# Kernel tuning notes

Hardware: AMD Instinct MI355X
Metric: run time of the kernel (lower is better)

## Reference

```python
import jax, jax.numpy as jnp
import numpy as np

EPS = 1e-12  # layer_norm_eps

def gelu_bert(x):
    return 0.5 * x * (1.0 + jax.lax.erf(x / jnp.sqrt(2.0).astype(x.dtype)))

def sym_normalize(A):
    # D^{-1/2} A D^{-1/2} via outer-product scaling (algebraic form of diag matmuls)
    d = A.sum(-1)                      # [B,N] row sums
    dinv = jnp.power(d, -0.5)
    return A * dinv[..., :, None] * dinv[..., None, :]

def layernorm(x, g, b):
    mu = x.mean(-1, keepdims=True)
    var = ((x - mu) ** 2).mean(-1, keepdims=True)
    return (x - mu) * jax.lax.rsqrt(var + EPS) * g + b

def gcn(x, adj, w1, w2):
    x = jax.nn.relu(jnp.matmul(adj, x @ w1))   # [B,N,I]
    x = jax.nn.relu(jnp.matmul(adj, x @ w2))   # [B,N,H]
    return x

def setup_inputs() -> dict:
    B, N, H, I = 8, 1024, 768, 3072
    key = jax.random.key(0)
    ks = jax.random.split(key, 20)
    s = 0.02
    inp = {
        'nodes': jax.random.normal(ks[0], (B, N, H), jnp.float32),
        'graphs': jax.random.uniform(ks[1], (B, 2, N, N), jnp.float32),
        'gcn1_w1': jax.random.normal(ks[2], (H, I), jnp.float32) * s,
        'gcn1_w2': jax.random.normal(ks[3], (I, H), jnp.float32) * s,
        'gcn2_w1': jax.random.normal(ks[4], (H, I), jnp.float32) * s,
        'gcn2_w2': jax.random.normal(ks[5], (I, H), jnp.float32) * s,
        'exp1_w': jax.random.normal(ks[6], (H, I), jnp.float32) * s,
        'exp1_b': jnp.zeros((I,), jnp.float32),
        'col1_w': jax.random.normal(ks[7], (I, H), jnp.float32) * s,
        'col1_b': jnp.zeros((H,), jnp.float32),
        'exp2_w': jax.random.normal(ks[8], (H, I), jnp.float32) * s,
        'exp2_b': jnp.zeros((I,), jnp.float32),
        'col2_w': jax.random.normal(ks[9], (I, H), jnp.float32) * s,
        'col2_b': jnp.zeros((H,), jnp.float32),
        'gate_w': jax.random.normal(ks[10], (4 * H, H), jnp.float32) * s,
        'gate_b': jnp.zeros((H,), jnp.float32),
        'ln1_g': jnp.ones((H,), jnp.float32),
        'ln1_b': jnp.zeros((H,), jnp.float32),
        'ln2_g': jnp.ones((H,), jnp.float32),
        'ln2_b': jnp.zeros((H,), jnp.float32),
    }
    return inp

def reference(nodes, graphs, gcn1_w1, gcn1_w2, gcn2_w1, gcn2_w2,
              exp1_w, exp1_b, col1_w, col1_b, exp2_w, exp2_b, col2_w, col2_b,
              gate_w, gate_b, ln1_g, ln1_b, ln2_g, ln2_b):
    adj1 = sym_normalize(graphs[:, 0])   # [B,N,N]
    adj2 = sym_normalize(graphs[:, 1])
    g1 = gcn(nodes, adj1, gcn1_w1, gcn1_w2)  # [B,N,H]
    g2 = gcn(nodes, adj2, gcn2_w1, gcn2_w2)
    # FFN + residual + LN (dropout = identity at eval)
    g1 = gelu_bert(g1 @ exp1_w + exp1_b) @ col1_w + col1_b
    g1 = layernorm(nodes + g1, ln1_g, ln1_b)
    g2 = gelu_bert(g2 @ exp2_w + exp2_b) @ col2_w + col2_b
    g2 = layernorm(nodes + g2, ln2_g, ln2_b)
    gate_in = jnp.concatenate((g1, g2, g1 + g2, g1 - g2), axis=2)  # [B,N,4H]
    gate = jax.nn.sigmoid(gate_in @ gate_w + gate_b)
    return gate * g1 + (1.0 - gate) * g2
```

## Files before the change

kernel.cpp:

```cpp
#include <hip/hip_runtime.h>
#include <hip/hip_bf16.h>

typedef __bf16 b8v __attribute__((ext_vector_type(8)));
typedef float  f4v __attribute__((ext_vector_type(4)));
typedef unsigned long long ull;

#define AS3(p)  ((__attribute__((address_space(3))) void*)(p))
#define AS1C(p) ((const __attribute__((address_space(1))) void*)(p))

template<int EPI>
__global__ __launch_bounds__(512, 2) void gemm256(
    const __hip_bfloat16* __restrict__ A,  long long sA,
    const __hip_bfloat16* __restrict__ Bt, long long sBg, long long sBb, int ldB,
    __hip_bfloat16* __restrict__ C, long long sC, int ldC,
    const float* __restrict__ bias0, const float* __restrict__ bias1, int K)
{
  const int bz = blockIdx.z;
  A  += (long long)bz * sA;
  Bt += (long long)(bz >> 3) * sBg + (long long)(bz & 7) * sBb;
  const float* __restrict__ bias = (bz & 1) ? bias1 : bias0;

  __shared__ __hip_bfloat16 As[4][8192];
  __shared__ __hip_bfloat16 Bs[4][8192];

  const int tid  = threadIdx.x;
  const int lane = tid & 63;
  const int wave = tid >> 6;
  const int wr = wave >> 2;
  const int wc = wave & 3;
  const int lm = lane & 15;
  const int kq = lane >> 4;

  const long long m0 = (long long)blockIdx.x * 256;
  const long long n0 = (long long)blockIdx.y * 256;

  const int sr  = tid >> 2;
  const int gch = (tid & 3) ^ ((tid >> 3) & 3);
  const __hip_bfloat16* aRow = A  + (m0 + sr) * (long long)K   + gch * 8;
  const __hip_bfloat16* bRow = Bt + (n0 + sr) * (long long)ldB + gch * 8;
  const int ld0 = tid * 8;

  auto stage = [&](int t) {
    const int buf = t & 3, k0 = t * 32;
    __builtin_amdgcn_global_load_lds(AS1C(aRow + k0),               AS3(&As[buf][ld0]),        16, 0, 0);
    __builtin_amdgcn_global_load_lds(AS1C(aRow + k0 + 128LL * K),   AS3(&As[buf][4096 + ld0]), 16, 0, 0);
    __builtin_amdgcn_global_load_lds(AS1C(bRow + k0),               AS3(&Bs[buf][ld0]),        16, 0, 0);
    __builtin_amdgcn_global_load_lds(AS1C(bRow + k0 + 128LL * ldB), AS3(&Bs[buf][4096 + ld0]), 16, 0, 0);
  };

  const int NK = K >> 5;
  stage(0); stage(1); stage(2);

  f4v acc[8][4];
  const f4v fz = {0.0f, 0.0f, 0.0f, 0.0f};
#pragma unroll
  for (int i = 0; i < 8; i++)
#pragma unroll
    for (int j = 0; j < 4; j++) acc[i][j] = fz;

  const int swz  = (kq ^ ((lm >> 1) & 3)) * 8;
  const int aoff = (wr * 128 + lm) * 32 + swz;
  const int boff = (wc * 64  + lm) * 32 + swz;

#define GBODY(T, VM)                                                          \
  {                                                                           \
    asm volatile("s_waitcnt vmcnt(" #VM ")" ::: "memory");                    \
    __builtin_amdgcn_s_barrier();                                             \
    __builtin_amdgcn_sched_barrier(0);                                        \
    if ((T) + 3 < NK) stage((T) + 3);                                         \
    const int buf_ = (T) & 3;                                                 \
    b8v af[8], bf[4];                                                         \
    _Pragma("unroll")                                                         \
    for (int i = 0; i < 8; i++) af[i] = *(const b8v*)(&As[buf_][aoff + i * 512]); \
    _Pragma("unroll")                                                         \
    for (int j = 0; j < 4; j++) bf[j] = *(const b8v*)(&Bs[buf_][boff + j * 512]); \
    __builtin_amdgcn_s_setprio(1);                                            \
    _Pragma("unroll")                                                         \
    for (int i = 0; i < 8; i++)                                               \
      _Pragma("unroll")                                                       \
      for (int j = 0; j < 4; j++)                                             \
        acc[i][j] = __builtin_amdgcn_mfma_f32_16x16x32_bf16(bf[j], af[i], acc[i][j], 0, 0, 0); \
    __builtin_amdgcn_s_setprio(0);                                            \
  }

  for (int t = 0; t < NK - 2; ++t) GBODY(t, 8)
  GBODY(NK - 2, 4)
  GBODY(NK - 1, 0)
#undef GBODY

#pragma unroll
  for (int i = 0; i < 8; i++) {
    const long long row = m0 + wr * 128 + i * 16 + lm;
#pragma unroll
    for (int j = 0; j < 4; j++) {
      const int colb = (int)n0 + wc * 64 + j * 16 + kq * 4;
      float v[4];
#pragma unroll
      for (int rg = 0; rg < 4; rg++) v[rg] = acc[i][j][rg];
      if constexpr (EPI == 1) {
#pragma unroll
        for (int rg = 0; rg < 4; rg++) v[rg] = fmaxf(v[rg], 0.0f);
      }
      if constexpr (EPI == 2) {
        const float4 b4 = *(const float4*)(bias + colb);
        const float* bb = (const float*)&b4;
#pragma unroll
        for (int rg = 0; rg < 4; rg++) {
          float x = v[rg] + bb[rg];
          v[rg] = 0.5f * x * (1.0f + erff(x * 0.70710678118654752f));
        }
      }
      union { __hip_bfloat16 h[4]; ull u; } P;
#pragma unroll
      for (int rg = 0; rg < 4; rg++) P.h[rg] = __float2bfloat16(v[rg]);
      *(ull*)(C + (long long)bz * sC + row * (long long)ldC + colb) = P.u;
    }
  }
}

template<int EPI, int OBF, int ORIENT, int MP>
__global__ __launch_bounds__(256) void gemm_bt(
    const __hip_bfloat16* __restrict__ A,  long long sA,
    const __hip_bfloat16* __restrict__ Bt, long long sBg, long long sBb, int ldB,
    void* __restrict__ Cv, long long sC, int ldC,
    const float* __restrict__ bias0, const float* __restrict__ bias1,
    const __hip_bfloat16* __restrict__ gcat, int K)
{
  const int bz = blockIdx.z;
  A  += (long long)bz * sA;
  Bt += (long long)(bz >> 3) * sBg + (long long)(bz & 7) * sBb;
  const float* __restrict__ bias = (bz & 1) ? bias1 : bias0;

  __shared__ __hip_bfloat16 As[128 * 32];
  __shared__ __hip_bfloat16 Bs[128 * 32];

  const int tid  = threadIdx.x;
  const int lane = tid & 63;
  const int wave = tid >> 6;

  const long long mBase = (long long)blockIdx.x * (MP * 128);
  const long long n0    = (long long)blockIdx.y * 128;

  const int r  = tid >> 2;
  const int kc = (tid & 3) ^ ((r >> 2) & 3);
  const __hip_bfloat16* aRow = A  + (mBase + r) * (long long)K   + kc * 8;
  const __hip_bfloat16* bRow = Bt + (n0 + r)    * (long long)ldB + kc * 8;

  const int wm = (wave & 1) * 64;
  const int wn = (wave >> 1) * 64;
  const int lm = lane & 15;
  const int kq = lane >> 4;

  const int sw   = (lm >> 2) & 3;
  const int aOff = (wm + lm) * 32 + (kq ^ sw) * 8;
  const int bOff = (wn + lm) * 32 + (kq ^ sw) * 8;

  auto stage = [&](long long aoff, int k0) {
    const __hip_bfloat16* a = aRow + aoff + k0;
    const __hip_bfloat16* b = bRow + k0;
    __builtin_amdgcn_global_load_lds(AS1C(a),              AS3(As + tid * 8),        16, 0, 0);
    __builtin_amdgcn_global_load_lds(AS1C(a + 64LL * K),   AS3(As + 2048 + tid * 8), 16, 0, 0);
    __builtin_amdgcn_global_load_lds(AS1C(b),              AS3(Bs + tid * 8),        16, 0, 0);
    __builtin_amdgcn_global_load_lds(AS1C(b + 64LL * ldB), AS3(Bs + 2048 + tid * 8), 16, 0, 0);
  };

  stage(0, 0);

  const f4v fzero = {0.0f, 0.0f, 0.0f, 0.0f};
  char* Cb = (char*)Cv;

  for (int p = 0; p < MP; ++p) {
    const long long aoff = (long long)p * 128 * K;

    f4v acc[4][4];
#pragma unroll
    for (int i = 0; i < 4; i++)
#pragma unroll
      for (int j = 0; j < 4; j++) acc[i][j] = fzero;

    for (int k0 = 0; k0 < K; k0 += 32) {
      __syncthreads();

      b8v af[4], bf[4];
#pragma unroll
      for (int i = 0; i < 4; i++) af[i] = *(const b8v*)(As + aOff + i * 16 * 32);
#pragma unroll
      for (int j = 0; j < 4; j++) bf[j] = *(const b8v*)(Bs + bOff + j * 16 * 32);

      __syncthreads();

      if (k0 + 32 < K)            stage(aoff, k0 + 32);
      else if (MP > 1 && p + 1 < MP) stage(aoff + 128LL * K, 0);

#pragma unroll
      for (int i = 0; i < 4; i++)
#pragma unroll
        for (int j = 0; j < 4; j++) {
          if constexpr (ORIENT == 0)
            acc[i][j] = __builtin_amdgcn_mfma_f32_16x16x32_bf16(bf[j], af[i], acc[i][j], 0, 0, 0);
          else
            acc[i][j] = __builtin_amdgcn_mfma_f32_16x16x32_bf16(af[i], bf[j], acc[i][j], 0, 0, 0);
        }
    }

    const long long m0 = mBase + (long long)p * 128;
#pragma unroll
    for (int i = 0; i < 4; i++) {
#pragma unroll
      for (int j = 0; j < 4; j++) {
        float v[4];
#pragma unroll
        for (int rg = 0; rg < 4; rg++) v[rg] = acc[i][j][rg];

        if constexpr (ORIENT == 0) {
          const long long row  = m0 + wm + i * 16 + lm;
          const int       colb = (int)n0 + wn + j * 16 + kq * 4;
          if constexpr (EPI == 1) {
#pragma unroll
            for (int rg = 0; rg < 4; rg++) v[rg] = fmaxf(v[rg], 0.0f);
          }
          if constexpr (EPI == 2) {
            const float4 b4 = *(const float4*)(bias + colb);
            const float* bb = (const float*)&b4;
#pragma unroll
            for (int rg = 0; rg < 4; rg++) {
              float x = v[rg] + bb[rg];
              v[rg] = 0.5f * x * (1.0f + erff(x * 0.70710678118654752f));
            }
          }
          const long long base = bz * sC + row * (long long)ldC + colb;
          if constexpr (EPI == 3) {
            const float4 b4 = *(const float4*)(bias0 + colb);
            const float* bb = (const float*)&b4;
            union { __hip_bfloat16 h[4]; ull u; } g1, g2;
            g1.u = *(const ull*)(gcat + row * 1536 + colb);
            g2.u = *(const ull*)(gcat + row * 1536 + 768 + colb);
            float o[4];
#pragma unroll
            for (int rg = 0; rg < 4; rg++) {
              const float s = 1.0f / (1.0f + expf(-(v[rg] + bb[rg])));
              o[rg] = s * __bfloat162float(g1.h[rg]) +
                      (1.0f - s) * __bfloat162float(g2.h[rg]);
            }
            *(float4*)(Cb + base * 4) = *(const float4*)o;
          } else if constexpr (OBF) {
            union { __hip_bfloat16 h[4]; ull u; } P;
#pragma unroll
            for (int rg = 0; rg < 4; rg++) P.h[rg] = __float2bfloat16(v[rg]);
            *(ull*)(Cb + base * 2) = P.u;
          } else {
            *(float4*)(Cb + base * 4) = *(const float4*)v;
          }
        } else {
          const long long crow = n0 + wn + j * 16 + lm;
          const long long mb   = m0 + wm + i * 16 + kq * 4;
          if constexpr (EPI == 1) {
#pragma unroll
            for (int rg = 0; rg < 4; rg++) v[rg] = fmaxf(v[rg], 0.0f);
          }
          const long long base = bz * sC + crow * (long long)ldC + mb;
          if constexpr (OBF) {
            union { __hip_bfloat16 h[4]; ull u; } P;
#pragma unroll
            for (int rg = 0; rg < 4; rg++) P.h[rg] = __float2bfloat16(v[rg]);
            *(ull*)(Cb + base * 2) = P.u;
          } else {
            *(float4*)(Cb + base * 4) = *(const float4*)v;
          }
        }
      }
    }
  }
}

__global__ __launch_bounds__(256) void rowsum_dinv(const float* __restrict__ g,
                                                   float* __restrict__ dinv)
{
  const int wave = threadIdx.x >> 6, lane = threadIdx.x & 63;
  const long long row = (long long)blockIdx.x * 4 + wave;
  const float4* p = (const float4*)(g + row * 1024);
  float s = 0.0f;
#pragma unroll
  for (int k = 0; k < 4; k++) {
    float4 v = p[lane + k * 64];
    s += v.x + v.y + v.z + v.w;
  }
#pragma unroll
  for (int o = 32; o > 0; o >>= 1) s += __shfl_down(s, o);
  if (lane == 0) dinv[row] = 1.0f / sqrtf(s);
}

__global__ __launch_bounds__(256) void scale_adj(const float* __restrict__ g,
                                                 const float* __restrict__ dinv,
                                                 __hip_bfloat16* __restrict__ out)
{
  const long long t = (long long)blockIdx.x * 256 + threadIdx.x;
  const long long e = t * 4;
  const int m = (int)(e >> 20);
  const int i = (int)((e >> 10) & 1023);
  const int j = (int)(e & 1023);
  const float4 v  = *(const float4*)(g + e);
  const float  di = dinv[m * 1024 + i];
  const float4 dj = *(const float4*)(dinv + m * 1024 + j);
  const int om = (m & 1) * 8 + (m >> 1);
  union { __hip_bfloat16 h[4]; ull u; } r;
  r.h[0] = __float2bfloat16(v.x * di * dj.x);
  r.h[1] = __float2bfloat16(v.y * di * dj.y);
  r.h[2] = __float2bfloat16(v.z * di * dj.z);
  r.h[3] = __float2bfloat16(v.w * di * dj.w);
  *(ull*)(out + ((long long)om << 20) + (long long)i * 1024 + j) = r.u;
}

template<typename TIN>
__global__ void transpose_conv(const TIN* __restrict__ in, __hip_bfloat16* __restrict__ out,
                               int R, int C, long long sIn, long long sOut)
{
  __shared__ __hip_bfloat16 tile[32][33];
  in  += (long long)blockIdx.z * sIn;
  out += (long long)blockIdx.z * sOut;
  const int c0 = blockIdx.x * 32, r0 = blockIdx.y * 32;
  const int tx = threadIdx.x, ty = threadIdx.y;
#pragma unroll
  for (int i = 0; i < 32; i += 8)
    tile[ty + i][tx] = __float2bfloat16((float)in[(long long)(r0 + ty + i) * C + c0 + tx]);
  __syncthreads();
#pragma unroll
  for (int i = 0; i < 32; i += 8)
    out[(long long)(c0 + ty + i) * R + r0 + tx] = tile[tx][ty + i];
}

__global__ __launch_bounds__(256) void ln_residual2(
    const float* __restrict__ nodes, const __hip_bfloat16* __restrict__ V,
    const float* __restrict__ colb0, const float* __restrict__ colb1,
    const float* __restrict__ lng0,  const float* __restrict__ lng1,
    const float* __restrict__ lnb0,  const float* __restrict__ lnb1,
    __hip_bfloat16* __restrict__ gcat)
{
  const long long row = blockIdx.x;
  const int g = (int)(row >> 13);
  const long long rr = row & 8191;
  const float* __restrict__ colb = g ? colb1 : colb0;
  const float* __restrict__ lng  = g ? lng1  : lng0;
  const float* __restrict__ lnb  = g ? lnb1  : lnb0;
  const int t = threadIdx.x;
  const long long nbase = rr * 768;
  const long long vbase = row * 768;
  float x[3]; float s = 0.0f, ss = 0.0f;
#pragma unroll
  for (int i = 0; i < 3; i++) {
    const int c = t + i * 256;
    const float v = nodes[nbase + c] + __bfloat162float(V[vbase + c]) + colb[c];
    x[i] = v; s += v; ss += v * v;
  }
  __shared__ float red[8];
#pragma unroll
  for (int o = 32; o > 0; o >>= 1) { s += __shfl_down(s, o); ss += __shfl_down(ss, o); }
  const int wave = t >> 6, lane = t & 63;
  if (lane == 0) { red[wave] = s; red[4 + wave] = ss; }
  __syncthreads();
  if (t == 0) {
    red[0] = red[0] + red[1] + red[2] + red[3];
    red[4] = red[4] + red[5] + red[6] + red[7];
  }
  __syncthreads();
  const float mu  = red[0] * (1.0f / 768.0f);
  float var = red[4] * (1.0f / 768.0f) - mu * mu;
  var = fmaxf(var, 0.0f);
  const float rs = rsqrtf(var + 1e-12f);
#pragma unroll
  for (int i = 0; i < 3; i++) {
    const int c = t + i * 256;
    const float y = (x[i] - mu) * rs * lng[c] + lnb[c];
    gcat[rr * 1536 + g * 768 + c] = __float2bfloat16(y);
  }
}

__global__ __launch_bounds__(256) void build_wefft(const float* __restrict__ gw,
                                                   __hip_bfloat16* __restrict__ wt)
{
  const int idx = blockIdx.x * 256 + threadIdx.x;
  const int n = idx / 1536, k = idx % 1536;
  float v;
  if (k < 768) v = gw[k * 768 + n] + gw[(1536 + k) * 768 + n] + gw[(2304 + k) * 768 + n];
  else {
    const int kk = k - 768;
    v = gw[(768 + kk) * 768 + n] + gw[(1536 + kk) * 768 + n] - gw[(2304 + kk) * 768 + n];
  }
  wt[idx] = __float2bfloat16(v);
}

extern "C" void kernel_launch(void* const* d_in, const int* in_sizes, int n_in,
                              void* d_out, int out_size, void* d_ws, size_t ws_size,
                              hipStream_t stream)
{
  const float* nodes  = (const float*)d_in[0];
  const float* graphs = (const float*)d_in[1];
  const float* gcn_w1[2] = { (const float*)d_in[2], (const float*)d_in[4] };
  const float* gcn_w2[2] = { (const float*)d_in[3], (const float*)d_in[5] };
  const float* exp_w[2]  = { (const float*)d_in[6],  (const float*)d_in[10] };
  const float* exp_b[2]  = { (const float*)d_in[7],  (const float*)d_in[11] };
  const float* col_w[2]  = { (const float*)d_in[8],  (const float*)d_in[12] };
  const float* col_b[2]  = { (const float*)d_in[9],  (const float*)d_in[13] };
  const float* gate_w = (const float*)d_in[14];
  const float* gate_b = (const float*)d_in[15];
  const float* ln_g[2] = { (const float*)d_in[16], (const float*)d_in[18] };
  const float* ln_b[2] = { (const float*)d_in[17], (const float*)d_in[19] };
  float* out = (float*)d_out;

  char* w = (char*)d_ws;
  auto alloc = [&](size_t bytes) { char* p = w; w += (bytes + 255) & ~(size_t)255; return p; };
  float*          dinv   = (float*)alloc(16384ULL * 4);
  char*           regA   = alloc(16ULL * 1024 * 1024 * 2);
  __hip_bfloat16* adj2   = (__hip_bfloat16*)regA;
  __hip_bfloat16* Gcat   = (__hip_bfloat16*)regA;
  __hip_bfloat16* wefft  = (__hip_bfloat16*)alloc(768ULL * 1536 * 2);
  __hip_bfloat16* bufA2  = (__hip_bfloat16*)alloc(16ULL * 1024 * 768 * 2);
  char*           regD   = alloc(16ULL * 1024 * 768 * 2);
  __hip_bfloat16* Xt     = (__hip_bfloat16*)regD;
  __hip_bfloat16* bufB2  = (__hip_bfloat16*)regD;
  __hip_bfloat16* X12    = (__hip_bfloat16*)alloc(2ULL * 8192 * 3072 * 2);
  __hip_bfloat16* wgt1   = (__hip_bfloat16*)alloc(2ULL * 3072 * 768 * 2);
  __hip_bfloat16* wgt2   = (__hip_bfloat16*)alloc(2ULL * 768 * 3072 * 2);

  const long long sW1 = 3072LL * 768;
  const long long sW2 = 768LL * 3072;
  const long long sNM = 1024LL * 768;
  const long long sBig = 8192LL * 3072;

  rowsum_dinv<<<4096, 256, 0, stream>>>(graphs, dinv);
  transpose_conv<float><<<dim3(24, 32, 8), dim3(32, 8), 0, stream>>>(
      nodes, Xt, 1024, 768, 1024LL * 768, 768LL * 1024);
  build_wefft<<<4608, 256, 0, stream>>>(gate_w, wefft);
  scale_adj<<<16384, 256, 0, stream>>>(graphs, dinv, adj2);
  for (int g = 0; g < 2; g++) {
    transpose_conv<float><<<dim3(96, 24, 1), dim3(32, 8), 0, stream>>>(
        gcn_w1[g], wgt1 + g * sW1, 768, 3072, 0, 0);
    transpose_conv<float><<<dim3(24, 96, 1), dim3(32, 8), 0, stream>>>(
        gcn_w2[g], wgt2 + g * sW2, 3072, 768, 0, 0);
  }

  gemm256<0><<<dim3(4, 3, 16), 512, 0, stream>>>(
      adj2, 1LL << 20, Xt, 0, sNM, 1024, bufA2, sNM, 768,
      nullptr, nullptr, 1024);
  gemm256<1><<<dim3(32, 12, 2), 512, 0, stream>>>(
      bufA2, 8192LL * 768, wgt1, 0, sW1, 768, X12, sBig, 3072,
      nullptr, nullptr, 768);
  gemm256<0><<<dim3(3, 32, 2), 512, 0, stream>>>(
      wgt2, sW2, X12, 0, sBig, 3072, bufA2, 768LL * 8192, 8192,
      nullptr, nullptr, 3072);
  for (int g = 0; g < 2; g++) {
    transpose_conv<float><<<dim3(96, 24, 1), dim3(32, 8), 0, stream>>>(
        exp_w[g], wgt1 + g * sW1, 768, 3072, 0, 0);
    transpose_conv<float><<<dim3(24, 96, 1), dim3(32, 8), 0, stream>>>(
        col_w[g], wgt2 + g * sW2, 3072, 768, 0, 0);
  }
  gemm256<1><<<dim3(4, 3, 16), 512, 0, stream>>>(
      adj2, 1LL << 20, bufA2, 768LL * 8192, 1024, 8192, bufB2, sNM, 768,
      nullptr, nullptr, 1024);
  gemm256<2><<<dim3(32, 12, 2), 512, 0, stream>>>(
      bufB2, 8192LL * 768, wgt1, 0, sW1, 768, X12, sBig, 3072,
      exp_b[0], exp_b[1], 768);
  gemm256<0><<<dim3(32, 3, 2), 512, 0, stream>>>(
      X12, sBig, wgt2, 0, sW2, 3072, bufA2, 8192LL * 768, 768,
      nullptr, nullptr, 3072);
  ln_residual2<<<16384, 256, 0, stream>>>(
      nodes, bufA2, col_b[0], col_b[1], ln_g[0], ln_g[1], ln_b[0], ln_b[1], Gcat);
  gemm_bt<3, 0, 0, 1><<<dim3(64, 6, 1), 256, 0, stream>>>(
      Gcat, 0, wefft, 0, 0, 1536, out, 0, 768,
      gate_b, nullptr, Gcat, 1536);
}
```

Measured before the change: 900.2 us.

## Split GEMM K-step into two half-phases interleaving A/B prefetch with MFMA

Each K-iteration of the 256x256 GEMM main loop is split into two phases. The first loads half of the A fragments plus the B fragments and issues the A prefetch. The second loads the other half of A and issues the B prefetch. Extra barriers and lgkmcnt waits separate LDS reads from the MFMA blocks. The aim is to interleave global-to-LDS staging with compute so the two waves per SIMD can ping-pong, and to cut register pressure from fragments. The cost is four barriers per K-step instead of one, which can add sync stalls.

Result: faster. 822.6 us (-8.6%).

```diff
diff --git a/kernel.cpp b/kernel.cpp
--- a/kernel.cpp
+++ b/kernel.cpp
@@ -40,16 +40,19 @@
   const __hip_bfloat16* bRow = Bt + (n0 + sr) * (long long)ldB + gch * 8;
   const int ld0 = tid * 8;
 
-  auto stage = [&](int t) {
+  auto stageA = [&](int t) {
     const int buf = t & 3, k0 = t * 32;
     __builtin_amdgcn_global_load_lds(AS1C(aRow + k0),               AS3(&As[buf][ld0]),        16, 0, 0);
     __builtin_amdgcn_global_load_lds(AS1C(aRow + k0 + 128LL * K),   AS3(&As[buf][4096 + ld0]), 16, 0, 0);
+  };
+  auto stageB = [&](int t) {
+    const int buf = t & 3, k0 = t * 32;
     __builtin_amdgcn_global_load_lds(AS1C(bRow + k0),               AS3(&Bs[buf][ld0]),        16, 0, 0);
     __builtin_amdgcn_global_load_lds(AS1C(bRow + k0 + 128LL * ldB), AS3(&Bs[buf][4096 + ld0]), 16, 0, 0);
   };
 
   const int NK = K >> 5;
-  stage(0); stage(1); stage(2);
+  stageA(0); stageB(0); stageA(1); stageB(1); stageA(2); stageB(2);
 
   f4v acc[8][4];
   const f4v fz = {0.0f, 0.0f, 0.0f, 0.0f};
@@ -62,31 +65,54 @@
   const int aoff = (wr * 128 + lm) * 32 + swz;
   const int boff = (wc * 64  + lm) * 32 + swz;
 
-#define GBODY(T, VM)                                                          \
+#define GSTEP(T, VM)                                                          \
   {                                                                           \
     asm volatile("s_waitcnt vmcnt(" #VM ")" ::: "memory");                    \
+    __builtin_amdgcn_s_barrier();                        \
+    __builtin_amdgcn_sched_barrier(0);                                        \
+    const int buf_ = (T) & 3;                                                 \
+    b8v afL[4], afH[4], bf[4];                                                \
+                    \
+    _Pragma("unroll")                                                         \
+    for (int i = 0; i < 4; i++) afL[i] = *(const b8v*)(&As[buf_][aoff + i * 512]); \
+    _Pragma("unroll")                                                         \
+    for (int j = 0; j < 4; j++) bf[j]  = *(const b8v*)(&Bs[buf_][boff + j * 512]); \
+    if ((T) + 3 < NK) stageA((T) + 3);                                        \
+    __builtin_amdgcn_sched_barrier(0);                                        \
     __builtin_amdgcn_s_barrier();                                             \
-    __builtin_amdgcn_sched_barrier(0);                                        \
-    if ((T) + 3 < NK) stage((T) + 3);                                         \
-    const int buf_ = (T) & 3;                                                 \
-    b8v af[8], bf[4];                                                         \
-    _Pragma("unroll")                                                         \
-    for (int i = 0; i < 8; i++) af[i] = *(const b8v*)(&As[buf_][aoff + i * 512]); \
-    _Pragma("unroll")                                                         \
-    for (int j = 0; j < 4; j++) bf[j] = *(const b8v*)(&Bs[buf_][boff + j * 512]); \
+    asm volatile("s_waitcnt lgkmcnt(0)" ::: "memory");                        \
+    __builtin_amdgcn_sched_barrier(0);                                        \
     __builtin_amdgcn_s_setprio(1);                                            \
     _Pragma("unroll")                                                         \
-    for (int i = 0; i < 8; i++)                                               \
+    for (int i = 0; i < 4; i++)                                               \
       _Pragma("unroll")                                                       \
       for (int j = 0; j < 4; j++)                                             \
-        acc[i][j] = __builtin_amdgcn_mfma_f32_16x16x32_bf16(bf[j], af[i], acc[i][j], 0, 0, 0); \
+        acc[i][j] = __builtin_amdgcn_mfma_f32_16x16x32_bf16(bf[j], afL[i], acc[i][j], 0, 0, 0); \
     __builtin_amdgcn_s_setprio(0);                                            \
-  }
-
-  for (int t = 0; t < NK - 2; ++t) GBODY(t, 8)
-  GBODY(NK - 2, 4)
-  GBODY(NK - 1, 0)
-#undef GBODY
+    __builtin_amdgcn_sched_barrier(0);                                        \
+    __builtin_amdgcn_s_barrier();                                             \
+                    \
+    _Pragma("unroll")                                                         \
+    for (int i = 0; i < 4; i++) afH[i] = *(const b8v*)(&As[buf_][aoff + (4 + i) * 512]); \
+    if ((T) + 3 < NK) stageB((T) + 3);                                        \
+    __builtin_amdgcn_sched_barrier(0);                                        \
+    __builtin_amdgcn_s_barrier();                                             \
+    asm volatile("s_waitcnt lgkmcnt(0)" ::: "memory");                        \
+    __builtin_amdgcn_sched_barrier(0);                                        \
+    __builtin_amdgcn_s_setprio(1);                                            \
+    _Pragma("unroll")                                                         \
+    for (int i = 0; i < 4; i++)                                               \
+      _Pragma("unroll")                                                       \
+      for (int j = 0; j < 4; j++)                                             \
+        acc[4 + i][j] = __builtin_amdgcn_mfma_f32_16x16x32_bf16(bf[j], afH[i], acc[4 + i][j], 0, 0, 0); \
+    __builtin_amdgcn_s_setprio(0);                                            \
+    __builtin_amdgcn_sched_barrier(0);                                        \
+  }
+
+  for (int t = 0; t < NK - 2; ++t) GSTEP(t, 8)
+  GSTEP(NK - 2, 4)
+  GSTEP(NK - 1, 0)
+#undef GSTEP
 
 #pragma unroll
   for (int i = 0; i < 8; i++) {
```

## Restructure GEMM main loop into BK=64 double-buffered four-phase ping-pong schedule

Applied to the files above, without the earlier changes.

Replaces the 4-stage BK=32 LDS ring with a double-buffered BK=64 layout split into half-tiles. Each K step runs four MFMA quadrants, and the next tile's A/B halves are staged between quadrants as each LDS region is freed. A new 8-chunk XOR swizzle matches the 64-wide rows. The goal is finer interleaving of global-to-LDS copies with MFMA work and fewer loop iterations, at the cost of more barriers per iteration and only double buffering.

New measurement: 803.8 us. 10.7% less time.

```diff
diff --git a/kernel.cpp b/kernel.cpp
--- a/kernel.cpp
+++ b/kernel.cpp
@@ -7,6 +7,7 @@
 
 #define AS3(p)  ((__attribute__((address_space(3))) void*)(p))
 #define AS1C(p) ((const __attribute__((address_space(1))) void*)(p))
+#define MFMA16(a, b, c) __builtin_amdgcn_mfma_f32_16x16x32_bf16((a), (b), (c), 0, 0, 0)
 
 template<int EPI>
 __global__ __launch_bounds__(512, 2) void gemm256(
@@ -20,8 +21,8 @@
   Bt += (long long)(bz >> 3) * sBg + (long long)(bz & 7) * sBb;
   const float* __restrict__ bias = (bz & 1) ? bias1 : bias0;
 
-  __shared__ __hip_bfloat16 As[4][8192];
-  __shared__ __hip_bfloat16 Bs[4][8192];
+  __shared__ __hip_bfloat16 As[2][2][8192];
+  __shared__ __hip_bfloat16 Bs[2][2][8192];
 
   const int tid  = threadIdx.x;
   const int lane = tid & 63;
@@ -34,22 +35,27 @@
   const long long m0 = (long long)blockIdx.x * 256;
   const long long n0 = (long long)blockIdx.y * 256;
 
-  const int sr  = tid >> 2;
-  const int gch = (tid & 3) ^ ((tid >> 3) & 3);
-  const __hip_bfloat16* aRow = A  + (m0 + sr) * (long long)K   + gch * 8;
-  const __hip_bfloat16* bRow = Bt + (n0 + sr) * (long long)ldB + gch * 8;
-  const int ld0 = tid * 8;
-
-  auto stage = [&](int t) {
-    const int buf = t & 3, k0 = t * 32;
-    __builtin_amdgcn_global_load_lds(AS1C(aRow + k0),               AS3(&As[buf][ld0]),        16, 0, 0);
-    __builtin_amdgcn_global_load_lds(AS1C(aRow + k0 + 128LL * K),   AS3(&As[buf][4096 + ld0]), 16, 0, 0);
-    __builtin_amdgcn_global_load_lds(AS1C(bRow + k0),               AS3(&Bs[buf][ld0]),        16, 0, 0);
-    __builtin_amdgcn_global_load_lds(AS1C(bRow + k0 + 128LL * ldB), AS3(&Bs[buf][4096 + ld0]), 16, 0, 0);
+  const int sr  = tid >> 3;
+  const int sc  = tid & 7;
+  const int gch = sc ^ (sr & 7);
+  const int ldsE = tid * 8;
+
+  auto stageA = [&](int d, int h, int kt) {
+    const __hip_bfloat16* s0 = A + (m0 + h * 128 + sr) * (long long)K + (long long)kt * 64 + gch * 8;
+    __builtin_amdgcn_global_load_lds(AS1C(s0),            AS3(&As[d][h][ldsE]),        16, 0, 0);
+    __builtin_amdgcn_global_load_lds(AS1C(s0 + 64LL * K), AS3(&As[d][h][4096 + ldsE]), 16, 0, 0);
   };
-
-  const int NK = K >> 5;
-  stage(0); stage(1); stage(2);
+  auto stageB = [&](int d, int h, int kt) {
+    const __hip_bfloat16* s0 = Bt + (n0 + h * 128 + sr) * (long long)ldB + (long long)kt * 64 + gch * 8;
+    __builtin_amdgcn_global_load_lds(AS1C(s0),              AS3(&Bs[d][h][ldsE]),        16, 0, 0);
+    __builtin_amdgcn_global_load_lds(AS1C(s0 + 64LL * ldB), AS3(&Bs[d][h][4096 + ldsE]), 16, 0, 0);
+  };
+
+  const int NT = K >> 6;
+  stageA(0, 0, 0); stageA(0, 1, 0); stageB(0, 0, 0); stageB(0, 1, 0);
+  stageA(1, 0, 1);
+  asm volatile("s_waitcnt vmcnt(2)" ::: "memory");
+  __builtin_amdgcn_s_barrier();
 
   f4v acc[8][4];
   const f4v fz = {0.0f, 0.0f, 0.0f, 0.0f};
@@ -58,35 +64,100 @@
 #pragma unroll
     for (int j = 0; j < 4; j++) acc[i][j] = fz;
 
-  const int swz  = (kq ^ ((lm >> 1) & 3)) * 8;
-  const int aoff = (wr * 128 + lm) * 32 + swz;
-  const int boff = (wc * 64  + lm) * 32 + swz;
-
-#define GBODY(T, VM)                                                          \
-  {                                                                           \
-    asm volatile("s_waitcnt vmcnt(" #VM ")" ::: "memory");                    \
-    __builtin_amdgcn_s_barrier();                                             \
-    __builtin_amdgcn_sched_barrier(0);                                        \
-    if ((T) + 3 < NK) stage((T) + 3);                                         \
-    const int buf_ = (T) & 3;                                                 \
-    b8v af[8], bf[4];                                                         \
-    _Pragma("unroll")                                                         \
-    for (int i = 0; i < 8; i++) af[i] = *(const b8v*)(&As[buf_][aoff + i * 512]); \
-    _Pragma("unroll")                                                         \
-    for (int j = 0; j < 4; j++) bf[j] = *(const b8v*)(&Bs[buf_][boff + j * 512]); \
-    __builtin_amdgcn_s_setprio(1);                                            \
-    _Pragma("unroll")                                                         \
-    for (int i = 0; i < 8; i++)                                               \
-      _Pragma("unroll")                                                       \
-      for (int j = 0; j < 4; j++)                                             \
-        acc[i][j] = __builtin_amdgcn_mfma_f32_16x16x32_bf16(bf[j], af[i], acc[i][j], 0, 0, 0); \
-    __builtin_amdgcn_s_setprio(0);                                            \
-  }
-
-  for (int t = 0; t < NK - 2; ++t) GBODY(t, 8)
-  GBODY(NK - 2, 4)
-  GBODY(NK - 1, 0)
-#undef GBODY
+  const int rb  = lm * 64;
+  const int cs0 = ((kq)     ^ (lm & 7)) * 8;
+  const int cs1 = ((4 + kq) ^ (lm & 7)) * 8;
+
+  for (int kt = 0; kt < NT; ++kt) {
+    const int d = kt & 1, dn = d ^ 1;
+    const __hip_bfloat16* Ab = &As[d][wr][0];
+    const __hip_bfloat16* Bb = &Bs[d][wc >> 1][(wc & 1) * 4096];
+    const bool st1 = (kt + 1 < NT);
+    b8v afL[8], afH[8], bfL[4], bfH[4];
+
+#pragma unroll
+    for (int f = 0; f < 4; f++) {
+      afL[f * 2]     = *(const b8v*)(Ab + f * 1024 + rb + cs0);
+      afL[f * 2 + 1] = *(const b8v*)(Ab + f * 1024 + rb + cs1);
+    }
+#pragma unroll
+    for (int f = 0; f < 2; f++) {
+      bfL[f * 2]     = *(const b8v*)(Bb + f * 1024 + rb + cs0);
+      bfL[f * 2 + 1] = *(const b8v*)(Bb + f * 1024 + rb + cs1);
+    }
+    if (st1) stageA(dn, 1, kt + 1);
+    __builtin_amdgcn_s_barrier();
+    asm volatile("s_waitcnt lgkmcnt(0)" ::: "memory");
+    __builtin_amdgcn_sched_barrier(0);
+    __builtin_amdgcn_s_setprio(1);
+#pragma unroll
+    for (int i = 0; i < 4; i++)
+#pragma unroll
+      for (int j = 0; j < 2; j++) acc[i][j] = MFMA16(bfL[j * 2], afL[i * 2], acc[i][j]);
+#pragma unroll
+    for (int i = 0; i < 4; i++)
+#pragma unroll
+      for (int j = 0; j < 2; j++) acc[i][j] = MFMA16(bfL[j * 2 + 1], afL[i * 2 + 1], acc[i][j]);
+    __builtin_amdgcn_s_setprio(0);
+    __builtin_amdgcn_s_barrier();
+
+#pragma unroll
+    for (int f = 0; f < 2; f++) {
+      bfH[f * 2]     = *(const b8v*)(Bb + (2 + f) * 1024 + rb + cs0);
+      bfH[f * 2 + 1] = *(const b8v*)(Bb + (2 + f) * 1024 + rb + cs1);
+    }
+    if (st1) stageB(dn, 0, kt + 1);
+    __builtin_amdgcn_s_barrier();
+    asm volatile("s_waitcnt lgkmcnt(0)" ::: "memory");
+    __builtin_amdgcn_sched_barrier(0);
+    __builtin_amdgcn_s_setprio(1);
+#pragma unroll
+    for (int i = 0; i < 4; i++)
+#pragma unroll
+      for (int j = 0; j < 2; j++) acc[i][2 + j] = MFMA16(bfH[j * 2], afL[i * 2], acc[i][2 + j]);
+#pragma unroll
+    for (int i = 0; i < 4; i++)
+#pragma unroll
+      for (int j = 0; j < 2; j++) acc[i][2 + j] = MFMA16(bfH[j * 2 + 1], afL[i * 2 + 1], acc[i][2 + j]);
+    __builtin_amdgcn_s_setprio(0);
+    __builtin_amdgcn_s_barrier();
+
+#pragma unroll
+    for (int f = 0; f < 4; f++) {
+      afH[f * 2]     = *(const b8v*)(Ab + (4 + f) * 1024 + rb + cs0);
+      afH[f * 2 + 1] = *(const b8v*)(Ab + (4 + f) * 1024 + rb + cs1);
+    }
+    if (st1) stageB(dn, 1, kt + 1);
+    __builtin_amdgcn_s_barrier();
+    asm volatile("s_waitcnt lgkmcnt(0)" ::: "memory");
+    __builtin_amdgcn_sched_barrier(0);
+    __builtin_amdgcn_s_setprio(1);
+#pragma unroll
+    for (int i = 0; i < 4; i++)
+#pragma unroll
+      for (int j = 0; j < 2; j++) acc[4 + i][j] = MFMA16(bfL[j * 2], afH[i * 2], acc[4 + i][j]);
+#pragma unroll
+    for (int i = 0; i < 4; i++)
+#pragma unroll
+      for (int j = 0; j < 2; j++) acc[4 + i][j] = MFMA16(bfL[j * 2 + 1], afH[i * 2 + 1], acc[4 + i][j]);
+    __builtin_amdgcn_s_setprio(0);
+    __builtin_amdgcn_s_barrier();
+
+    if (kt + 2 < NT) stageA(d, 0, kt + 2);
+    __builtin_amdgcn_s_setprio(1);
+#pragma unroll
+    for (int i = 0; i < 4; i++)
+#pragma unroll
+      for (int j = 0; j < 2; j++) acc[4 + i][2 + j] = MFMA16(bfH[j * 2], afH[i * 2], acc[4 + i][2 + j]);
+#pragma unroll
+    for (int i = 0; i < 4; i++)
+#pragma unroll
+      for (int j = 0; j < 2; j++) acc[4 + i][2 + j] = MFMA16(bfH[j * 2 + 1], afH[i * 2 + 1], acc[4 + i][2 + j]);
+    __builtin_amdgcn_s_setprio(0);
+    if (kt + 2 < NT) asm volatile("s_waitcnt vmcnt(2)" ::: "memory");
+    else             asm volatile("s_waitcnt vmcnt(0)" ::: "memory");
+    __builtin_amdgcn_s_barrier();
+  }
 
 #pragma unroll
   for (int i = 0; i < 8; i++) {
```
